# Performance work log

Hardware: AMD Instinct MI355X
Metric: run time of the kernel (lower is better)

## Reference

```python
import jax, jax.numpy as jnp
import numpy as np
from jax import lax

N = 4667      # num vertices (hardcoded in Spatial_Attention_layer)
B = 4         # batch
T = 8         # raw timesteps; (T-2)*3 == 18 after TimeBlock + concat
C_IN = 2      # input features
TP = 18       # concatenated timesteps
HID = 16      # TimeBlock out channels / PCN fc width
N_ROOTS = 500
BRANCH = 2
DEPTH = 3


def _build_tree():
    # Static stand-in for the P/roots/s2rDic dict-based trajectory tree.
    rng = np.random.RandomState(42)
    roots = rng.choice(N, N_ROOTS, replace=False)
    path_node = [int(r) for r in roots]
    levels = []
    prev = list(range(N_ROOTS))
    for _ in range(DEPTH):
        p_idx, c_idx, pn, cn, nxt = [], [], [], [], []
        for pi in prev:
            kids = rng.choice(N, BRANCH, replace=False)
            for c in kids:
                ci = len(path_node)
                path_node.append(int(c))
                p_idx.append(pi); c_idx.append(ci)
                pn.append(path_node[pi]); cn.append(int(c))
                nxt.append(ci)
        levels.append((np.array(p_idx), np.array(c_idx), np.array(pn), np.array(cn)))
        prev = nxt
    leaf_idx = np.array(prev)
    leaf_node = np.array([path_node[i] for i in prev])
    return np.asarray(roots), levels, leaf_idx, leaf_node, len(path_node)

ROOTS, LEVELS, LEAF_IDX, LEAF_NODES, NUM_PATHS = _build_tree()
ROOT_PATH_IDX = np.arange(N_ROOTS)


def setup_inputs() -> dict:
    key = jax.random.key(0)
    ks = jax.random.split(key, 16)
    f = jnp.float32
    rn = lambda k, s: 0.1 * jax.random.normal(k, s, f)
    return {
        "X": jax.random.normal(ks[0], (B, N, T, C_IN), f),
        "X_daily": jax.random.normal(ks[1], (B, N, T, C_IN), f),
        "X_weekly": jax.random.normal(ks[2], (B, N, T, C_IN), f),
        "mask": jnp.zeros((1,), jnp.int32),  # unused in forward (as in source)
        "conv1_w": rn(ks[3], (HID, C_IN, 1, 3)),
        "conv1_b": rn(ks[4], (HID,)),
        "conv2_w": rn(ks[5], (HID, C_IN, 1, 3)),
        "conv2_b": rn(ks[6], (HID,)),
        "W1": rn(ks[7], (HID,)),
        "W2": rn(ks[8], (TP, HID)),
        "W3": rn(ks[9], (TP,)),
        "bs": rn(ks[10], (1, N, N)),
        "Vs": rn(ks[11], (N, N)),
        "fc_w": rn(ks[12], (HID, HID)),
        "fc_b": rn(ks[13], (HID,)),
    }


def reference(X, X_daily, X_weekly, mask, conv1_w, conv1_b, conv2_w, conv2_b,
              W1, W2, W3, bs, Vs, fc_w, fc_b):
    dn = ("NCHW", "OIHW", "NCHW")

    def time_block(Xin):
        # [B,N,T,C] -> [B,C,N,T] -> GLU conv over time -> [B,N,T-2,HID]
        Xp = jnp.transpose(Xin, (0, 3, 1, 2))
        c1 = lax.conv_general_dilated(Xp, conv1_w, (1, 1), "VALID", dimension_numbers=dn) + conv1_b[None, :, None, None]
        c2 = lax.conv_general_dilated(Xp, conv2_w, (1, 1), "VALID", dimension_numbers=dn) + conv2_b[None, :, None, None]
        return jnp.transpose(c1 * jax.nn.sigmoid(c2), (0, 2, 3, 1))

    x = jnp.concatenate([time_block(X), time_block(X_daily), time_block(X_weekly)], axis=2)  # [B,N,18,16]

    # spatial attention
    lhs = jnp.einsum("bnt,tc->bnc", jnp.einsum("bntc,c->bnt", x, W1), W2)   # [B,N,16]
    rhs = jnp.einsum("t,bntc->bnc", W3, x)                                    # [B,N,16]
    product = jnp.einsum("bnc,bmc->bnm", lhs, rhs)                            # [B,N,N]
    S = jnp.einsum("nm,bmk->bnk", Vs, jax.nn.sigmoid(product + bs))           # [B,N,N]
    A = jax.nn.softmax(S, axis=1)

    # PCN tree propagation: h_child = fc(h_parent) * A[:, p, c] + x[c]
    xn = jnp.transpose(x, (1, 0, 2, 3))  # [N,B,18,16]
    H = jnp.zeros((NUM_PATHS, B, TP, HID), x.dtype)
    H = H.at[ROOT_PATH_IDX].set(xn[ROOTS])
    for p_idx, c_idx, pn, cn in LEVELS:
        hp = H[p_idx]                                   # [E,B,18,16]
        a = jnp.transpose(A[:, pn, cn])                 # [E,B]
        hc = (jnp.einsum("ebtc,dc->ebtd", hp, fc_w) + fc_b) * a[:, :, None, None] + xn[cn]
        H = H.at[c_idx].set(hc)

    # mean-pool leaf paths per terminal node; fall back to x for nodes w/o leaves
    leaf_h = H[LEAF_IDX]
    sums = jax.ops.segment_sum(leaf_h, LEAF_NODES, num_segments=N)
    counts = jax.ops.segment_sum(jnp.ones((LEAF_NODES.shape[0],), x.dtype), LEAF_NODES, num_segments=N)
    has_leaf = (counts > 0)[:, None, None, None]
    out_n = jnp.where(has_leaf, sums / jnp.maximum(counts, 1.0)[:, None, None, None], xn)
    return jnp.transpose(out_n, (1, 0, 2, 3))  # [B,N,18,16]
```

## Files before the change

### kernel.cpp

```cpp
#include <hip/hip_runtime.h>
#include <stdint.h>
#include <string.h>

#define NV      4667
#define BB      4
#define TT      8
#define TPX     18
#define HID     16
#define NROOTS  500
#define NPATHS  7500
#define NEDGES  7000
#define NLEAF   4000
#define NP2     4864
#define LDKQ    5120

typedef __bf16 bf16;
typedef bf16  bf16x4 __attribute__((ext_vector_type(4)));
typedef int   i32x4  __attribute__((ext_vector_type(4)));
typedef const void __attribute__((address_space(1))) gvoid;
typedef void       __attribute__((address_space(3))) svoid;

struct MT19937 {
    uint32_t mt[624]; int pos;
    void seed(uint32_t s) {
        for (int i = 0; i < 624; ++i) { mt[i] = s; s = 1812433253u * (s ^ (s >> 30)) + (uint32_t)i + 1u; }
        pos = 624;
    }
    uint32_t next() {
        if (pos >= 624) {
            for (int i = 0; i < 624; ++i) {
                uint32_t y = (mt[i] & 0x80000000u) | (mt[(i + 1) % 624] & 0x7fffffffu);
                uint32_t v = mt[(i + 397) % 624] ^ (y >> 1);
                if (y & 1u) v ^= 0x9908b0dfu;
                mt[i] = v;
            }
            pos = 0;
        }
        uint32_t y = mt[pos++];
        y ^= y >> 11; y ^= (y << 7) & 0x9d2c5680u; y ^= (y << 15) & 0xefc60000u; y ^= y >> 18;
        return y;
    }
    uint32_t interval(uint32_t mx) {
        if (!mx) return 0;
        uint32_t mask = mx;
        mask |= mask >> 1; mask |= mask >> 2; mask |= mask >> 4; mask |= mask >> 8; mask |= mask >> 16;
        uint32_t v;
        do { v = next() & mask; } while (v > mx);
        return v;
    }
};

struct TreeBlob {
    int path_node[NPATHS];
    int leaf_start[NV + 1];
    int leaf_path[NLEAF];
};

static void build_tree_host(TreeBlob* tb) {
    MT19937 rng; rng.seed(42);
    static int perm[NV];
    auto choice_take = [&](int* out, int k) {
        for (int i = 0; i < NV; ++i) perm[i] = i;
        for (int i = NV - 1; i >= 1; --i) {
            int j = (int)rng.interval((uint32_t)i);
            int t = perm[i]; perm[i] = perm[j]; perm[j] = t;
        }
        for (int i = 0; i < k; ++i) out[i] = perm[i];
    };
    int np_ = 0;
    int roots[NROOTS];
    choice_take(roots, NROOTS);
    for (int i = 0; i < NROOTS; ++i) tb->path_node[np_++] = roots[i];
    int prev_cnt = NROOTS;
    for (int lvl = 0; lvl < 3; ++lvl) {
        int kids[2];
        for (int p = 0; p < prev_cnt; ++p) {
            choice_take(kids, 2);
            tb->path_node[np_++] = kids[0];
            tb->path_node[np_++] = kids[1];
        }
        prev_cnt *= 2;
    }
    static int cnt[NV], cur[NV];
    memset(cnt, 0, sizeof(cnt));
    for (int l = 0; l < NLEAF; ++l) cnt[tb->path_node[3500 + l]]++;
    tb->leaf_start[0] = 0;
    for (int n = 0; n < NV; ++n) tb->leaf_start[n + 1] = tb->leaf_start[n] + cnt[n];
    for (int n = 0; n < NV; ++n) cur[n] = tb->leaf_start[n];
    for (int l = 0; l < NLEAF; ++l) {
        int n = tb->path_node[3500 + l];
        tb->leaf_path[cur[n]++] = 3500 + l;
    }
}

static TreeBlob* get_pinned_tree() {
    static TreeBlob* p = [] {
        TreeBlob* q = nullptr;
        if (hipHostMalloc((void**)&q, sizeof(TreeBlob), 0) != hipSuccess || !q) {
            static TreeBlob fallback;
            q = &fallback;
        }
        build_tree_host(q);
        return q;
    }();
    return p;
}

__global__ void k_timeblock(const float* __restrict__ X, const float* __restrict__ Xd,
                            const float* __restrict__ Xw,
                            const float* __restrict__ w1, const float* __restrict__ b1,
                            const float* __restrict__ w2, const float* __restrict__ b2,
                            float* __restrict__ x) {
    int idx = blockIdx.x * 256 + threadIdx.x;
    if (idx >= BB * NV * 18) return;
    int t = idx % 6;
    int g = (idx / 6) % 3;
    int n = (idx / 18) % NV;
    int b = idx / (18 * NV);
    const float* Xg = (g == 0) ? X : (g == 1) ? Xd : Xw;
    const float* p = Xg + (((size_t)b * NV + n) * TT + t) * 2;
    float v[6];
#pragma unroll
    for (int kk = 0; kk < 3; ++kk) { v[kk * 2 + 0] = p[kk * 2 + 0]; v[kk * 2 + 1] = p[kk * 2 + 1]; }
    float* xo = x + (((size_t)b * NV + n) * TPX + (g * 6 + t)) * HID;
#pragma unroll
    for (int o = 0; o < 16; ++o) {
        float c1 = b1[o], c2 = b2[o];
#pragma unroll
        for (int ci = 0; ci < 2; ++ci)
#pragma unroll
            for (int kk = 0; kk < 3; ++kk) {
                float xv = v[kk * 2 + ci];
                c1 += xv * w1[(o * 2 + ci) * 3 + kk];
                c2 += xv * w2[(o * 2 + ci) * 3 + kk];
            }
        xo[o] = c1 * (1.0f / (1.0f + __expf(-c2)));
    }
}

__global__ void k_lhsrhs(const float* __restrict__ x, const float* __restrict__ W1,
                         const float* __restrict__ W2, const float* __restrict__ W3,
                         float* __restrict__ lhs, float* __restrict__ rhs) {
    int idx = blockIdx.x * 256 + threadIdx.x;
    if (idx >= BB * NV) return;
    const float* xp = x + (size_t)idx * TPX * HID;
    float l[16], r[16];
#pragma unroll
    for (int c = 0; c < 16; ++c) { l[c] = 0.f; r[c] = 0.f; }
    for (int t = 0; t < TPX; ++t) {
        float xt = 0.f, w3 = W3[t];
#pragma unroll
        for (int c = 0; c < 16; ++c) { float xv = xp[t * 16 + c]; xt += xv * W1[c]; r[c] += w3 * xv; }
#pragma unroll
        for (int c = 0; c < 16; ++c) l[c] += xt * W2[t * 16 + c];
    }
    float* lo = lhs + (size_t)idx * 16;
    float* ro = rhs + (size_t)idx * 16;
#pragma unroll
    for (int c = 0; c < 16; ++c) { lo[c] = l[c]; ro[c] = r[c]; }
}

__global__ __launch_bounds__(256)
void k_vsq(const float* __restrict__ Vs, int8_t* __restrict__ Vq,
           float* __restrict__ sA, float* __restrict__ c0) {
    int n = blockIdx.x;
    int t = threadIdx.x;
    int8_t* row_out = Vq + (size_t)n * LDKQ;
    if (n >= NV) {
        for (int m = t * 4; m < LDKQ; m += 1024) *(int*)(row_out + m) = 0;
        if (t == 0) { sA[n] = 0.f; c0[n] = 0.f; }
        return;
    }
    const float* row = Vs + (size_t)n * NV;
    float mx = 0.f;
    for (int m = t; m < NV; m += 256) mx = fmaxf(mx, fabsf(row[m]));
#pragma unroll
    for (int o = 32; o; o >>= 1) mx = fmaxf(mx, __shfl_xor(mx, o));
    __shared__ float wred[4];
    __shared__ int ired[4];
    if ((t & 63) == 0) wred[t >> 6] = mx;
    __syncthreads();
    mx = fmaxf(fmaxf(wred[0], wred[1]), fmaxf(wred[2], wred[3]));
    mx = fmaxf(mx, 1e-30f);
    float inv = 127.f / mx;
    int qs = 0;
    for (int m0 = t * 4; m0 < LDKQ; m0 += 1024) {
        int pack = 0;
#pragma unroll
        for (int u = 0; u < 4; ++u) {
            int m = m0 + u;
            int q = 0;
            if (m < NV) q = (int)rintf(row[m] * inv);
            qs += q;
            pack |= (q & 0xff) << (8 * u);
        }
        *(int*)(row_out + m0) = pack;
    }
#pragma unroll
    for (int o = 32; o; o >>= 1) qs += __shfl_xor(qs, o);
    if ((t & 63) == 0) ired[t >> 6] = qs;
    __syncthreads();
    if (t == 0) {
        int tot = ired[0] + ired[1] + ired[2] + ired[3];
        sA[n] = mx / 32258.f;
        c0[n] = mx * (float)tot / 254.f;
    }
}

__global__ __launch_bounds__(256)
void k_sig(const float* __restrict__ lhs, const float* __restrict__ rhs,
           const float* __restrict__ bs, int8_t* __restrict__ Sq) {
    int m0 = blockIdx.x * 256;
    int k0 = blockIdx.y * 64;
    __shared__ bf16 bss[64 * 260];
    int t = threadIdx.x;

    for (int i = t; i < 256 * 64; i += 256) {
        int row = i >> 6, col = i & 63;
        int mg = m0 + row, kg = k0 + col;
        float v = (mg < NV && kg < NV) ? bs[(size_t)mg * NV + kg] : 0.f;
        bss[col * 260 + row] = (bf16)v;
    }
    __syncthreads();

    int ml = t & 63, kc = t >> 6;
    int mbase = m0 + ml * 4;

    for (int b = 0; b < BB; ++b) {
        float lv[4][16];
#pragma unroll
        for (int r = 0; r < 4; ++r) {
            int mg = mbase + r;
            if (mg < NV) {
                const float4* lp = (const float4*)&lhs[((size_t)b * NV + mg) * 16];
#pragma unroll
                for (int q = 0; q < 4; ++q) {
                    float4 f = lp[q];
                    lv[r][q * 4 + 0] = f.x; lv[r][q * 4 + 1] = f.y;
                    lv[r][q * 4 + 2] = f.z; lv[r][q * 4 + 3] = f.w;
                }
            } else {
#pragma unroll
                for (int c = 0; c < 16; ++c) lv[r][c] = 0.f;
            }
        }
#pragma unroll
        for (int kk = 0; kk < 16; ++kk) {
            int kl = kc * 16 + kk;
            int kg = k0 + kl;
            bool kvalid = (kg < NV);
            float rsv[16];
            if (kvalid) {
                const float4* rp = (const float4*)&rhs[((size_t)b * NV + kg) * 16];
#pragma unroll
                for (int q = 0; q < 4; ++q) {
                    float4 f = rp[q];
                    rsv[q * 4 + 0] = f.x; rsv[q * 4 + 1] = f.y;
                    rsv[q * 4 + 2] = f.z; rsv[q * 4 + 3] = f.w;
                }
            } else {
#pragma unroll
                for (int c = 0; c < 16; ++c) rsv[c] = 0.f;
            }
            bf16x4 bv = *(const bf16x4*)&bss[kl * 260 + ml * 4];
            int pack = 0;
#pragma unroll
            for (int r = 0; r < 4; ++r) {
                float dot = 0.f;
#pragma unroll
                for (int c = 0; c < 16; ++c) dot += lv[r][c] * rsv[c];
                float pv = dot + (float)bv[r];
                float s = 1.0f / (1.0f + __expf(-pv));
                int q = 0;
                if (kvalid && (mbase + r) < NV) q = (int)rintf(254.f * (s - 0.5f));
                pack |= (q & 0xff) << (8 * r);
            }
            *(int*)&Sq[((size_t)b * NP2 + kg) * LDKQ + mbase] = pack;
        }
    }
}

#define BUF0    0
#define BUF1    65536
#define A0OFF   0
#define A1OFF   16384
#define B0OFF   32768
#define B1OFF   49152

#define BARRIER() __builtin_amdgcn_s_barrier()
#define LGKM0()  asm volatile("s_waitcnt lgkmcnt(0)" ::: "memory")
#define LGKM8()  asm volatile("s_waitcnt lgkmcnt(8)" :::)
#define VM2()    asm volatile("s_waitcnt vmcnt(2)" ::: "memory")
#define VM4()    asm volatile("s_waitcnt vmcnt(4)" ::: "memory")
#define VM0()    asm volatile("s_waitcnt vmcnt(0)" ::: "memory")

#define DSA(buf, mh, mf, ks) (*(const i32x4*)(ldsb + (buf) + ((ks) ? aoff1 : aoff0) + (mh)*8192 + (mf)*2048))
#define DSB(buf, nf, ks)     (*(const i32x4*)(ldsb + (buf) + ((ks) ? boff1 : boff0) + (nf)*2048))

#define PH_READ_A(buf, mh) { \
    _Pragma("unroll") for (int mf = 0; mf < 4; ++mf) { \
        a[mf][0] = DSA(buf, mh, mf, 0); a[mf][1] = DSA(buf, mh, mf, 1); } }

#define PH_READ_B(buf, nh) { \
    _Pragma("unroll") for (int j = 0; j < 2; ++j) { \
        b[j][0] = DSB(buf, (nh)*2 + j, 0); b[j][1] = DSB(buf, (nh)*2 + j, 1); } }

#define PH_MMA(mh, nh) { \
    __builtin_amdgcn_s_setprio(1); \
    _Pragma("unroll") for (int mf = 0; mf < 4; ++mf) \
    _Pragma("unroll") for (int j = 0; j < 2; ++j) { \
        i32x4 c = acc[(mh)*4 + mf][(nh)*2 + j]; \
        c = __builtin_amdgcn_mfma_i32_16x16x64_i8(a[mf][0], b[j][0], c, 0, 0, 0); \
        c = __builtin_amdgcn_mfma_i32_16x16x64_i8(a[mf][1], b[j][1], c, 0, 0, 0); \
        acc[(mh)*4 + mf][(nh)*2 + j] = c; } \
    __builtin_amdgcn_s_setprio(0); }

#define STAGE(ldsoff, g, kt) { \
    const int8_t* _g = (g) + (size_t)(kt) * 128; \
    __builtin_amdgcn_global_load_lds((gvoid*)_g, (svoid*)(ldsb + (ldsoff) + dst0), 16, 0, 0); \
    __builtin_amdgcn_global_load_lds((gvoid*)(_g + (size_t)128 * LDKQ), (svoid*)(ldsb + (ldsoff) + dst0 + 8192), 16, 0, 0); }

__global__ __launch_bounds__(512, 2)
void k_gemm8(const int8_t* __restrict__ Vq, const int8_t* __restrict__ Sq,
             const float* __restrict__ sA, const float* __restrict__ c0,
             float* __restrict__ colsum) {
    extern __shared__ char ldsb[];

    int orig = blockIdx.x;
    int xcd = orig & 7, lin = orig >> 3;
    int wg = (xcd < 4) ? xcd * 181 + lin : 724 + (xcd - 4) * 180 + lin;
    int bi = wg % 19;
    int bk = (wg / 19) % 19;
    int bb = wg / 361;

    const int8_t* Aptr = Vq + (size_t)bi * 256 * LDKQ;
    const int8_t* Bptr = Sq + ((size_t)bb * NP2 + (size_t)bk * 256) * LDKQ;

    int t = threadIdx.x;
    int lane = t & 63, wv = t >> 6;
    int wr = wv >> 2, wc = wv & 3;
    int lr = lane & 15, lg = lane >> 4;
    int key = (lr & 7) << 4;

    int aoff0 = wr * 16384 + lr * 128 + ((lg * 16) ^ key);
    int aoff1 = wr * 16384 + lr * 128 + ((64 + lg * 16) ^ key);
    int boff0 = 32768 + (wc >> 1) * 16384 + ((wc & 1) * 64 + lr) * 128 + ((lg * 16) ^ key);
    int boff1 = 32768 + (wc >> 1) * 16384 + ((wc & 1) * 64 + lr) * 128 + ((64 + lg * 16) ^ key);

    int rl0 = t >> 3;
    int cb = (t & 7) << 4;
    int csw = cb ^ ((rl0 & 7) << 4);
    const int8_t* gA0 = Aptr + (size_t)rl0 * LDKQ + csw;
    const int8_t* gA1 = gA0 + (size_t)128 * LDKQ;
    const int8_t* gB0 = Bptr + (size_t)rl0 * LDKQ + csw;
    const int8_t* gB1 = gB0 + (size_t)128 * LDKQ;
    int dst0 = t * 16;

    i32x4 acc[8][4];
#pragma unroll
    for (int i = 0; i < 8; ++i)
#pragma unroll
        for (int j = 0; j < 4; ++j) acc[i][j] = i32x4{0, 0, 0, 0};

    i32x4 a[4][2], b[2][2];

    STAGE(BUF0 + B0OFF, gB0, 0);
    STAGE(BUF0 + B1OFF, gB1, 0);
    STAGE(BUF0 + A0OFF, gA0, 0);
    STAGE(BUF0 + A1OFF, gA1, 0);
    STAGE(BUF1 + A0OFF, gA0, 1);
    STAGE(BUF1 + A1OFF, gA1, 1);
    VM4();
    BARRIER();

    for (int i = 0; i < 19; ++i) {
        int t1 = 2 * i + 1, t2 = 2 * i + 2, t3 = 2 * i + 3;
        PH_READ_A(BUF0, 0); PH_READ_B(BUF0, 0);
        STAGE(BUF1 + B0OFF, gB0, t1);
        LGKM8();
        BARRIER(); LGKM0();
        PH_MMA(0, 0);
        BARRIER();
        PH_READ_B(BUF0, 1);
        STAGE(BUF1 + B1OFF, gB1, t1);
        BARRIER(); LGKM0();
        PH_MMA(0, 1);
        BARRIER();
        PH_READ_A(BUF0, 1);
        BARRIER(); LGKM0();
        PH_MMA(1, 1);
        BARRIER();
        PH_READ_B(BUF0, 0);
        STAGE(BUF0 + A0OFF, gA0, t2);
        BARRIER(); LGKM0();
        PH_MMA(1, 0);
        VM2();
        BARRIER();
        PH_READ_A(BUF1, 0); PH_READ_B(BUF1, 0);
        STAGE(BUF0 + A1OFF, gA1, t2);
        STAGE(BUF0 + B0OFF, gB0, t2);
        LGKM8();
        BARRIER(); LGKM0();
        PH_MMA(0, 0);
        BARRIER();
        PH_READ_B(BUF1, 1);
        STAGE(BUF0 + B1OFF, gB1, t2);
        BARRIER(); LGKM0();
        PH_MMA(0, 1);
        BARRIER();
        PH_READ_A(BUF1, 1);
        BARRIER(); LGKM0();
        PH_MMA(1, 1);
        BARRIER();
        PH_READ_B(BUF1, 0);
        STAGE(BUF1 + A0OFF, gA0, t3);
        STAGE(BUF1 + A1OFF, gA1, t3);
        BARRIER(); LGKM0();
        PH_MMA(1, 0);
        VM4();
        BARRIER();
    }
    VM0();

#pragma unroll
    for (int nj = 0; nj < 4; ++nj) {
        int col = bk * 256 + wc * 64 + nj * 16 + lr;
        float csum = 0.f;
#pragma unroll
        for (int mi = 0; mi < 8; ++mi) {
            int rowb = bi * 256 + wr * 128 + (mi >> 2) * 64 + (mi & 3) * 16 + lg * 4;
            float4 sa4 = *(const float4*)&sA[rowb];
            float4 c04 = *(const float4*)&c0[rowb];
            float sar[4] = {sa4.x, sa4.y, sa4.z, sa4.w};
            float c0r[4] = {c04.x, c04.y, c04.z, c04.w};
#pragma unroll
            for (int r = 0; r < 4; ++r) {
                float S = sar[r] * (float)acc[mi][nj][r] + c0r[r];
                csum += ((rowb + r) < NV && col < NV) ? __expf(S) : 0.f;
            }
        }
        csum += __shfl_xor(csum, 16);
        csum += __shfl_xor(csum, 32);
        if (lane < 16 && col < NV) atomicAdd(&colsum[(size_t)bb * NV + col], csum);
    }
}

__global__ void k_edge(const int8_t* __restrict__ Vq, const int8_t* __restrict__ Sq,
                       const float* __restrict__ sA, const float* __restrict__ c0,
                       const float* __restrict__ colsum, const int* __restrict__ path_node,
                       float* __restrict__ a_edge) {
    int g = blockIdx.x;
    int b = threadIdx.x >> 6;
    int lane = threadIdx.x & 63;
    int e, pbase, cbase;
    if (g < 1000)      { e = g;        pbase = 0;    cbase = 500;  }
    else if (g < 3000) { e = g - 1000; pbase = 500;  cbase = 1500; }
    else               { e = g - 3000; pbase = 1500; cbase = 3500; }
    int pn = path_node[pbase + (e >> 1)];
    int cn = path_node[cbase + e];
    const int8_t* va = Vq + (size_t)pn * LDKQ;
    const int8_t* vb = Sq + ((size_t)b * NP2 + cn) * LDKQ;
    int acc = 0;
    for (int i = lane * 16; i < LDKQ; i += 1024) {
        i32x4 a4 = *(const i32x4*)(va + i);
        i32x4 b4 = *(const i32x4*)(vb + i);
#pragma unroll
        for (int w = 0; w < 4; ++w) {
            int aw = a4[w], bw = b4[w];
#pragma unroll
            for (int q = 0; q < 4; ++q)
                acc += (int)(int8_t)(aw >> (8 * q)) * (int)(int8_t)(bw >> (8 * q));
        }
    }
#pragma unroll
    for (int o = 32; o; o >>= 1) acc += __shfl_xor(acc, o);
    if (lane == 0) {
        float S = sA[pn] * (float)acc + c0[pn];
        a_edge[(size_t)g * BB + b] = __expf(S) / colsum[(size_t)b * NV + cn];
    }
}

__global__ void k_root(const float* __restrict__ x, const int* __restrict__ path_node,
                       float* __restrict__ H) {
    int idx = blockIdx.x * 256 + threadIdx.x;
    if (idx >= NROOTS * BB * 288) return;
    int d = idx % 288;
    int b = (idx / 288) % BB;
    int p = idx / (288 * BB);
    int n = path_node[p];
    H[((size_t)p * BB + b) * 288 + d] = x[((size_t)b * NV + n) * 288 + d];
}

__global__ void k_level(const float* __restrict__ x, const int* __restrict__ path_node,
                        const float* __restrict__ fcw, const float* __restrict__ fcb,
                        const float* __restrict__ a_edge, float* __restrict__ H,
                        int E, int pbase, int cbase, int gbase) {
    int idx = blockIdx.x * 256 + threadIdx.x;
    if (idx >= E * BB * 288) return;
    int d = idx & 15;
    int t = (idx >> 4) % TPX;
    int b = (idx / (16 * TPX)) % BB;
    int e = idx / (16 * TPX * BB);
    int pp = pbase + (e >> 1);
    int cp = cbase + e;
    const float* hp = &H[(((size_t)pp * BB + b) * TPX + t) * HID];
    float acc = fcb[d];
#pragma unroll
    for (int c = 0; c < 16; ++c) acc += hp[c] * fcw[d * 16 + c];
    float a = a_edge[(size_t)(gbase + e) * BB + b];
    int cn = path_node[cp];
    float xv = x[(((size_t)b * NV + cn) * TPX + t) * HID + d];
    H[(((size_t)cp * BB + b) * TPX + t) * HID + d] = acc * a + xv;
}

__global__ void k_pool(const float* __restrict__ x, const float* __restrict__ H,
                       const int* __restrict__ leaf_start, const int* __restrict__ leaf_path,
                       float* __restrict__ out) {
    int n = blockIdx.x;
    int s = leaf_start[n], epos = leaf_start[n + 1];
    int cnt = epos - s;
    for (int idx = threadIdx.x; idx < BB * 288; idx += 256) {
        int b = idx / 288, d = idx % 288;
        float v;
        if (cnt == 0) {
            v = x[((size_t)b * NV + n) * 288 + d];
        } else {
            float sum = 0.f;
            for (int l = s; l < epos; ++l) {
                int p = leaf_path[l];
                sum += H[((size_t)p * BB + b) * 288 + d];
            }
            v = sum / (float)cnt;
        }
        out[((size_t)b * NV + n) * 288 + d] = v;
    }
}

extern "C" void kernel_launch(void* const* d_in, const int* in_sizes, int n_in,
                              void* d_out, int out_size, void* d_ws, size_t ws_size,
                              hipStream_t stream) {
    const float* X   = (const float*)d_in[0];
    const float* Xd  = (const float*)d_in[1];
    const float* Xw  = (const float*)d_in[2];
    const float* c1w = (const float*)d_in[4];
    const float* c1b = (const float*)d_in[5];
    const float* c2w = (const float*)d_in[6];
    const float* c2b = (const float*)d_in[7];
    const float* W1  = (const float*)d_in[8];
    const float* W2  = (const float*)d_in[9];
    const float* W3  = (const float*)d_in[10];
    const float* bs  = (const float*)d_in[11];
    const float* Vs  = (const float*)d_in[12];
    const float* fcw = (const float*)d_in[13];
    const float* fcb = (const float*)d_in[14];
    float* out = (float*)d_out;

    TreeBlob* pinned = get_pinned_tree();

    char* w = (char*)d_ws;
    auto alloc = [&](size_t bytes) { char* p = w; w += (bytes + 255) & ~(size_t)255; return p; };
    float*  x      = (float*)alloc((size_t)BB * NV * 288 * 4);
    float*  lhs    = (float*)alloc((size_t)BB * NV * 16 * 4);
    float*  rhs    = (float*)alloc((size_t)BB * NV * 16 * 4);
    float*  colsum = (float*)alloc((size_t)BB * NV * 4);
    float*  aedge  = (float*)alloc((size_t)NEDGES * BB * 4);
    float*  H      = (float*)alloc((size_t)NPATHS * BB * 288 * 4);
    float*  sAr    = (float*)alloc((size_t)NP2 * 4);
    float*  c0r    = (float*)alloc((size_t)NP2 * 4);
    int*    dtree  = (int*)alloc(sizeof(TreeBlob));
    int8_t* Vq     = (int8_t*)alloc((size_t)NP2 * LDKQ);
    int8_t* Sq     = (int8_t*)alloc((size_t)BB * NP2 * LDKQ);

    int* d_path   = dtree;
    int* d_lstart = dtree + NPATHS;
    int* d_lpath  = d_lstart + (NV + 1);

    hipFuncSetAttribute((const void*)k_gemm8, hipFuncAttributeMaxDynamicSharedMemorySize, 131072);

    hipMemcpyAsync(dtree, pinned, sizeof(TreeBlob), hipMemcpyHostToDevice, stream);
    hipMemsetAsync(colsum, 0, (size_t)BB * NV * 4, stream);

    k_timeblock<<<(BB * NV * 18 + 255) / 256, 256, 0, stream>>>(X, Xd, Xw, c1w, c1b, c2w, c2b, x);
    k_lhsrhs<<<(BB * NV + 255) / 256, 256, 0, stream>>>(x, W1, W2, W3, lhs, rhs);
    k_vsq<<<NP2, 256, 0, stream>>>(Vs, Vq, sAr, c0r);
    dim3 sgrid(LDKQ / 256, NP2 / 64);
    k_sig<<<sgrid, 256, 0, stream>>>(lhs, rhs, bs, Sq);
    k_gemm8<<<19 * 19 * BB, 512, 131072, stream>>>(Vq, Sq, sAr, c0r, colsum);
    k_edge<<<NEDGES, 256, 0, stream>>>(Vq, Sq, sAr, c0r, colsum, d_path, aedge);
    k_root<<<(NROOTS * BB * 288 + 255) / 256, 256, 0, stream>>>(x, d_path, H);
    k_level<<<(1000 * BB * 288 + 255) / 256, 256, 0, stream>>>(x, d_path, fcw, fcb, aedge, H, 1000, 0, 500, 0);
    k_level<<<(2000 * BB * 288 + 255) / 256, 256, 0, stream>>>(x, d_path, fcw, fcb, aedge, H, 2000, 500, 1500, 1000);
    k_level<<<(4000 * BB * 288 + 255) / 256, 256, 0, stream>>>(x, d_path, fcw, fcb, aedge, H, 4000, 1500, 3500, 3000);
    k_pool<<<NV, 256, 0, stream>>>(x, H, d_lstart, d_lpath, out);
}
```

Measured before the change: 829.5 us.

## Rewrite int8 GEMM with 32x32x32 MFMA and simpler double-buffered pipeline

Replaces the 16x16x64 int8 MFMA GEMM, with its fine-grained phased barrier schedule, by a 32x32x32 int8 MFMA version. The new version double-buffers whole 128-wide K windows in LDS with a single barrier per window. The epilogue is adapted to the 32x32 accumulator layout. Separately, the Vs quantization kernel now keeps each row in registers after the max pass instead of re-reading global memory, and writes bytes directly. The simpler pipeline waits for vmcnt(0) at each window, which may expose load latency that the previous interleaved schedule hid.

```diff
diff --git a/kernel.cpp b/kernel.cpp
--- a/kernel.cpp
+++ b/kernel.cpp
@@ -16,7 +16,8 @@
 
 typedef __bf16 bf16;
 typedef bf16  bf16x4 __attribute__((ext_vector_type(4)));
-typedef int   i32x4  __attribute__((ext_vector_type(4)));
+typedef int   i32x4v __attribute__((ext_vector_type(4)));
+typedef int   i32x16 __attribute__((ext_vector_type(16)));
 typedef const void __attribute__((address_space(1))) gvoid;
 typedef void       __attribute__((address_space(3))) svoid;
 
@@ -172,8 +173,14 @@
         return;
     }
     const float* row = Vs + (size_t)n * NV;
+    float v[20];
     float mx = 0.f;
-    for (int m = t; m < NV; m += 256) mx = fmaxf(mx, fabsf(row[m]));
+#pragma unroll
+    for (int i = 0; i < 20; ++i) {
+        int m = t + i * 256;
+        v[i] = (m < NV) ? row[m] : 0.f;
+        mx = fmaxf(mx, fabsf(v[i]));
+    }
 #pragma unroll
     for (int o = 32; o; o >>= 1) mx = fmaxf(mx, __shfl_xor(mx, o));
     __shared__ float wred[4];
@@ -184,17 +191,11 @@
     mx = fmaxf(mx, 1e-30f);
     float inv = 127.f / mx;
     int qs = 0;
-    for (int m0 = t * 4; m0 < LDKQ; m0 += 1024) {
-        int pack = 0;
-#pragma unroll
-        for (int u = 0; u < 4; ++u) {
-            int m = m0 + u;
-            int q = 0;
-            if (m < NV) q = (int)rintf(row[m] * inv);
-            qs += q;
-            pack |= (q & 0xff) << (8 * u);
-        }
-        *(int*)(row_out + m0) = pack;
+#pragma unroll
+    for (int i = 0; i < 20; ++i) {
+        int q = (int)rintf(v[i] * inv);
+        qs += q;
+        row_out[t + i * 256] = (int8_t)q;
     }
 #pragma unroll
     for (int o = 32; o; o >>= 1) qs += __shfl_xor(qs, o);
@@ -280,50 +281,44 @@
     }
 }
 
-#define BUF0    0
-#define BUF1    65536
-#define A0OFF   0
-#define A1OFF   16384
-#define B0OFF   32768
-#define B1OFF   49152
-
-#define BARRIER() __builtin_amdgcn_s_barrier()
-#define LGKM0()  asm volatile("s_waitcnt lgkmcnt(0)" ::: "memory")
-#define LGKM8()  asm volatile("s_waitcnt lgkmcnt(8)" :::)
-#define VM2()    asm volatile("s_waitcnt vmcnt(2)" ::: "memory")
-#define VM4()    asm volatile("s_waitcnt vmcnt(4)" ::: "memory")
-#define VM0()    asm volatile("s_waitcnt vmcnt(0)" ::: "memory")
-
-#define DSA(buf, mh, mf, ks) (*(const i32x4*)(ldsb + (buf) + ((ks) ? aoff1 : aoff0) + (mh)*8192 + (mf)*2048))
-#define DSB(buf, nf, ks)     (*(const i32x4*)(ldsb + (buf) + ((ks) ? boff1 : boff0) + (nf)*2048))
-
-#define PH_READ_A(buf, mh) { \
+#define STAGE4(dstoff, gptr, kt) { \
+    const int8_t* _g = (gptr) + (size_t)(kt) * 128; \
+    __builtin_amdgcn_global_load_lds((gvoid*)(_g),                     (svoid*)(sb + (dstoff) + dst0), 16, 0, 0); \
+    __builtin_amdgcn_global_load_lds((gvoid*)(_g + (size_t)64 * LDKQ), (svoid*)(sb + (dstoff) + dst0 + 8192), 16, 0, 0); \
+    __builtin_amdgcn_global_load_lds((gvoid*)(_g + (size_t)128 * LDKQ),(svoid*)(sb + (dstoff) + dst0 + 16384), 16, 0, 0); \
+    __builtin_amdgcn_global_load_lds((gvoid*)(_g + (size_t)192 * LDKQ),(svoid*)(sb + (dstoff) + dst0 + 24576), 16, 0, 0); }
+
+#define READ_G(ar, br, RB, K0) { \
     _Pragma("unroll") for (int mf = 0; mf < 4; ++mf) { \
-        a[mf][0] = DSA(buf, mh, mf, 0); a[mf][1] = DSA(buf, mh, mf, 1); } }
-
-#define PH_READ_B(buf, nh) { \
-    _Pragma("unroll") for (int j = 0; j < 2; ++j) { \
-        b[j][0] = DSB(buf, (nh)*2 + j, 0); b[j][1] = DSB(buf, (nh)*2 + j, 1); } }
-
-#define PH_MMA(mh, nh) { \
+        ar[mf][0] = *(const i32x4v*)((RB) + abase + mf * 4096 + colks[K0]); \
+        ar[mf][1] = *(const i32x4v*)((RB) + abase + mf * 4096 + colks[K0 + 1]); } \
+    _Pragma("unroll") for (int nf = 0; nf < 2; ++nf) { \
+        br[nf][0] = *(const i32x4v*)((RB) + bbase + nf * 4096 + colks[K0]); \
+        br[nf][1] = *(const i32x4v*)((RB) + bbase + nf * 4096 + colks[K0 + 1]); } }
+
+#define MMA_G(ar, br) { \
     __builtin_amdgcn_s_setprio(1); \
+    _Pragma("unroll") for (int kk = 0; kk < 2; ++kk) \
     _Pragma("unroll") for (int mf = 0; mf < 4; ++mf) \
-    _Pragma("unroll") for (int j = 0; j < 2; ++j) { \
-        i32x4 c = acc[(mh)*4 + mf][(nh)*2 + j]; \
-        c = __builtin_amdgcn_mfma_i32_16x16x64_i8(a[mf][0], b[j][0], c, 0, 0, 0); \
-        c = __builtin_amdgcn_mfma_i32_16x16x64_i8(a[mf][1], b[j][1], c, 0, 0, 0); \
-        acc[(mh)*4 + mf][(nh)*2 + j] = c; } \
+    _Pragma("unroll") for (int nf = 0; nf < 2; ++nf) \
+        acc[mf][nf] = __builtin_amdgcn_mfma_i32_32x32x32_i8(ar[mf][kk], br[nf][kk], acc[mf][nf], 0, 0, 0); \
     __builtin_amdgcn_s_setprio(0); }
 
-#define STAGE(ldsoff, g, kt) { \
-    const int8_t* _g = (g) + (size_t)(kt) * 128; \
-    __builtin_amdgcn_global_load_lds((gvoid*)_g, (svoid*)(ldsb + (ldsoff) + dst0), 16, 0, 0); \
-    __builtin_amdgcn_global_load_lds((gvoid*)(_g + (size_t)128 * LDKQ), (svoid*)(ldsb + (ldsoff) + dst0 + 8192), 16, 0, 0); }
+#define WINDOW(RB, SB, TSTAGE) { \
+    char* sb = (SB); \
+    STAGE4(0, gA, TSTAGE); \
+    STAGE4(32768, gB, TSTAGE); \
+    READ_G(a0, b0, RB, 0); \
+    READ_G(a1, b1, RB, 2); \
+    MMA_G(a0, b0); \
+    MMA_G(a1, b1); \
+    asm volatile("s_waitcnt vmcnt(0)" ::: "memory"); \
+    __builtin_amdgcn_s_barrier(); }
 
 __global__ __launch_bounds__(512, 2)
-void k_gemm8(const int8_t* __restrict__ Vq, const int8_t* __restrict__ Sq,
-             const float* __restrict__ sA, const float* __restrict__ c0,
-             float* __restrict__ colsum) {
+void k_gemm32(const int8_t* __restrict__ Vq, const int8_t* __restrict__ Sq,
+              const float* __restrict__ sA, const float* __restrict__ c0,
+              float* __restrict__ colsum) {
     extern __shared__ char ldsb[];
 
     int orig = blockIdx.x;
@@ -333,115 +328,69 @@
     int bk = (wg / 19) % 19;
     int bb = wg / 361;
 
-    const int8_t* Aptr = Vq + (size_t)bi * 256 * LDKQ;
-    const int8_t* Bptr = Sq + ((size_t)bb * NP2 + (size_t)bk * 256) * LDKQ;
-
     int t = threadIdx.x;
     int lane = t & 63, wv = t >> 6;
     int wr = wv >> 2, wc = wv & 3;
-    int lr = lane & 15, lg = lane >> 4;
-    int key = (lr & 7) << 4;
-
-    int aoff0 = wr * 16384 + lr * 128 + ((lg * 16) ^ key);
-    int aoff1 = wr * 16384 + lr * 128 + ((64 + lg * 16) ^ key);
-    int boff0 = 32768 + (wc >> 1) * 16384 + ((wc & 1) * 64 + lr) * 128 + ((lg * 16) ^ key);
-    int boff1 = 32768 + (wc >> 1) * 16384 + ((wc & 1) * 64 + lr) * 128 + ((64 + lg * 16) ^ key);
+    int l31 = lane & 31, hi = lane >> 5;
+    int key = (lane & 7) << 4;
+    int colks[4];
+#pragma unroll
+    for (int ks = 0; ks < 4; ++ks) colks[ks] = (ks * 32 + hi * 16) ^ key;
+    int abase = wr * 16384 + l31 * 128;
+    int bbase = 32768 + wc * 8192 + l31 * 128;
 
     int rl0 = t >> 3;
-    int cb = (t & 7) << 4;
-    int csw = cb ^ ((rl0 & 7) << 4);
-    const int8_t* gA0 = Aptr + (size_t)rl0 * LDKQ + csw;
-    const int8_t* gA1 = gA0 + (size_t)128 * LDKQ;
-    const int8_t* gB0 = Bptr + (size_t)rl0 * LDKQ + csw;
-    const int8_t* gB1 = gB0 + (size_t)128 * LDKQ;
+    int csw = ((t & 7) << 4) ^ ((rl0 & 7) << 4);
+    const int8_t* gA = Vq + ((size_t)(bi * 256) + rl0) * LDKQ + csw;
+    const int8_t* gB = Sq + ((size_t)bb * NP2 + (size_t)bk * 256 + rl0) * LDKQ + csw;
     int dst0 = t * 16;
 
-    i32x4 acc[8][4];
-#pragma unroll
-    for (int i = 0; i < 8; ++i)
-#pragma unroll
-        for (int j = 0; j < 4; ++j) acc[i][j] = i32x4{0, 0, 0, 0};
-
-    i32x4 a[4][2], b[2][2];
-
-    STAGE(BUF0 + B0OFF, gB0, 0);
-    STAGE(BUF0 + B1OFF, gB1, 0);
-    STAGE(BUF0 + A0OFF, gA0, 0);
-    STAGE(BUF0 + A1OFF, gA1, 0);
-    STAGE(BUF1 + A0OFF, gA0, 1);
-    STAGE(BUF1 + A1OFF, gA1, 1);
-    VM4();
-    BARRIER();
+    i32x16 acc[4][2];
+#pragma unroll
+    for (int i = 0; i < 4; ++i)
+#pragma unroll
+        for (int j = 0; j < 2; ++j)
+#pragma unroll
+            for (int r = 0; r < 16; ++r) acc[i][j][r] = 0;
+
+    i32x4v a0[4][2], a1[4][2], b0[2][2], b1[2][2];
+
+    {
+        char* sb = ldsb;
+        STAGE4(0, gA, 0);
+        STAGE4(32768, gB, 0);
+    }
+    asm volatile("s_waitcnt vmcnt(0)" ::: "memory");
+    __builtin_amdgcn_s_barrier();
 
     for (int i = 0; i < 19; ++i) {
-        int t1 = 2 * i + 1, t2 = 2 * i + 2, t3 = 2 * i + 3;
-        PH_READ_A(BUF0, 0); PH_READ_B(BUF0, 0);
-        STAGE(BUF1 + B0OFF, gB0, t1);
-        LGKM8();
-        BARRIER(); LGKM0();
-        PH_MMA(0, 0);
-        BARRIER();
-        PH_READ_B(BUF0, 1);
-        STAGE(BUF1 + B1OFF, gB1, t1);
-        BARRIER(); LGKM0();
-        PH_MMA(0, 1);
-        BARRIER();
-        PH_READ_A(BUF0, 1);
-        BARRIER(); LGKM0();
-        PH_MMA(1, 1);
-        BARRIER();
-        PH_READ_B(BUF0, 0);
-        STAGE(BUF0 + A0OFF, gA0, t2);
-        BARRIER(); LGKM0();
-        PH_MMA(1, 0);
-        VM2();
-        BARRIER();
-        PH_READ_A(BUF1, 0); PH_READ_B(BUF1, 0);
-        STAGE(BUF0 + A1OFF, gA1, t2);
-        STAGE(BUF0 + B0OFF, gB0, t2);
-        LGKM8();
-        BARRIER(); LGKM0();
-        PH_MMA(0, 0);
-        BARRIER();
-        PH_READ_B(BUF1, 1);
-        STAGE(BUF0 + B1OFF, gB1, t2);
-        BARRIER(); LGKM0();
-        PH_MMA(0, 1);
-        BARRIER();
-        PH_READ_A(BUF1, 1);
-        BARRIER(); LGKM0();
-        PH_MMA(1, 1);
-        BARRIER();
-        PH_READ_B(BUF1, 0);
-        STAGE(BUF1 + A0OFF, gA0, t3);
-        STAGE(BUF1 + A1OFF, gA1, t3);
-        BARRIER(); LGKM0();
-        PH_MMA(1, 0);
-        VM4();
-        BARRIER();
-    }
-    VM0();
-
-#pragma unroll
-    for (int nj = 0; nj < 4; ++nj) {
-        int col = bk * 256 + wc * 64 + nj * 16 + lr;
+        WINDOW(ldsb,         ldsb + 65536, 2 * i + 1);
+        WINDOW(ldsb + 65536, ldsb,         2 * i + 2);
+    }
+
+#pragma unroll
+    for (int nf = 0; nf < 2; ++nf) {
+        int col = bk * 256 + wc * 64 + nf * 32 + l31;
         float csum = 0.f;
 #pragma unroll
-        for (int mi = 0; mi < 8; ++mi) {
-            int rowb = bi * 256 + wr * 128 + (mi >> 2) * 64 + (mi & 3) * 16 + lg * 4;
-            float4 sa4 = *(const float4*)&sA[rowb];
-            float4 c04 = *(const float4*)&c0[rowb];
-            float sar[4] = {sa4.x, sa4.y, sa4.z, sa4.w};
-            float c0r[4] = {c04.x, c04.y, c04.z, c04.w};
-#pragma unroll
-            for (int r = 0; r < 4; ++r) {
-                float S = sar[r] * (float)acc[mi][nj][r] + c0r[r];
-                csum += ((rowb + r) < NV && col < NV) ? __expf(S) : 0.f;
-            }
-        }
-        csum += __shfl_xor(csum, 16);
+        for (int mf = 0; mf < 4; ++mf) {
+            int rowb = bi * 256 + wr * 128 + mf * 32 + 4 * hi;
+#pragma unroll
+            for (int g = 0; g < 4; ++g) {
+                int rg = rowb + 8 * g;
+                float4 sa4 = *(const float4*)&sA[rg];
+                float4 c04 = *(const float4*)&c0[rg];
+                float sar[4] = {sa4.x, sa4.y, sa4.z, sa4.w};
+                float c0r[4] = {c04.x, c04.y, c04.z, c04.w};
+#pragma unroll
+                for (int r = 0; r < 4; ++r) {
+                    float S = sar[r] * (float)acc[mf][nf][g * 4 + r] + c0r[r];
+                    csum += ((rg + r) < NV && col < NV) ? __expf(S) : 0.f;
+                }
+            }
+        }
         csum += __shfl_xor(csum, 32);
-        if (lane < 16 && col < NV) atomicAdd(&colsum[(size_t)bb * NV + col], csum);
+        if (lane < 32 && col < NV) atomicAdd(&colsum[(size_t)bb * NV + col], csum);
     }
 }
 
@@ -462,8 +411,8 @@
     const int8_t* vb = Sq + ((size_t)b * NP2 + cn) * LDKQ;
     int acc = 0;
     for (int i = lane * 16; i < LDKQ; i += 1024) {
-        i32x4 a4 = *(const i32x4*)(va + i);
-        i32x4 b4 = *(const i32x4*)(vb + i);
+        i32x4v a4 = *(const i32x4v*)(va + i);
+        i32x4v b4 = *(const i32x4v*)(vb + i);
 #pragma unroll
         for (int w = 0; w < 4; ++w) {
             int aw = a4[w], bw = b4[w];
@@ -575,7 +524,7 @@
     int* d_lstart = dtree + NPATHS;
     int* d_lpath  = d_lstart + (NV + 1);
 
-    hipFuncSetAttribute((const void*)k_gemm8, hipFuncAttributeMaxDynamicSharedMemorySize, 131072);
+    hipFuncSetAttribute((const void*)k_gemm32, hipFuncAttributeMaxDynamicSharedMemorySize, 131072);
 
     hipMemcpyAsync(dtree, pinned, sizeof(TreeBlob), hipMemcpyHostToDevice, stream);
     hipMemsetAsync(colsum, 0, (size_t)BB * NV * 4, stream);
@@ -585,7 +534,7 @@
     k_vsq<<<NP2, 256, 0, stream>>>(Vs, Vq, sAr, c0r);
     dim3 sgrid(LDKQ / 256, NP2 / 64);
     k_sig<<<sgrid, 256, 0, stream>>>(lhs, rhs, bs, Sq);
-    k_gemm8<<<19 * 19 * BB, 512, 131072, stream>>>(Vq, Sq, sAr, c0r, colsum);
+    k_gemm32<<<19 * 19 * BB, 512, 131072, stream>>>(Vq, Sq, sAr, c0r, colsum);
     k_edge<<<NEDGES, 256, 0, stream>>>(Vq, Sq, sAr, c0r, colsum, d_path, aedge);
     k_root<<<(NROOTS * BB * 288 + 255) / 256, 256, 0, stream>>>(x, d_path, H);
     k_level<<<(1000 * BB * 288 + 255) / 256, 256, 0, stream>>>(x, d_path, fcw, fcb, aedge, H, 1000, 0, 500, 0);
```

New measurement: 856.2 us. 3.2% more time.
